# Kernel tuning notes

Measured on AMD Instinct MI355X. Metric: run time of the kernel, lower is better.

Reference implementation:

```python
import jax, jax.numpy as jnp
import numpy as np

N_QUBITS = 12
N_LAYERS = 6
BATCH = 8192
D_IN = 512


def _apply_1q(state, gate, wire):
    # state: [B] + [2]*n (real), gate: [2,2]. new[j] = sum_i gate[j,i]*old[i]
    s = jnp.moveaxis(state, 1 + wire, -1)
    s = jnp.einsum('...i,ji->...j', s, gate)
    return jnp.moveaxis(s, -1, 1 + wire)


def _apply_cnot(state, ctrl, tgt):
    # flip target amplitude pair where control bit == 1
    s = jnp.moveaxis(state, (1 + ctrl, 1 + tgt), (-2, -1))
    s = jnp.concatenate([s[..., :1, :], s[..., 1:, ::-1]], axis=-2)
    return jnp.moveaxis(s, (-2, -1), (1 + ctrl, 1 + tgt))


def _simulate(angles, weights):
    # angles: [B, n] per-sample RY angles; weights: [L, n] shared RY angles.
    # Circuit: H + RY(angle) per wire on |0>, then L x (RY layer + CNOT chain).
    # All gates are real -> real float32 statevector.
    B, n = angles.shape
    L = weights.shape[0]
    inv_sqrt2 = jnp.float32(1.0 / np.sqrt(2.0))
    half = 0.5 * angles
    c, s = jnp.cos(half), jnp.sin(half)
    # per-wire single-qubit state RY(a) @ H @ |0> = inv_sqrt2 * [c-s, c+s]
    v = inv_sqrt2 * jnp.stack([c - s, c + s], axis=-1)  # [B, n, 2]
    state = v[:, 0]  # [B, 2]
    for w in range(1, n):
        state = jnp.einsum('b...,bj->b...j', state, v[:, w])  # product state
    # state: [B] + [2]*n
    for layer in range(L):
        h = 0.5 * weights[layer]
        cl, sl = jnp.cos(h), jnp.sin(h)
        for w in range(n):
            gate = jnp.stack([jnp.stack([cl[w], -sl[w]]),
                              jnp.stack([sl[w], cl[w]])])
            state = _apply_1q(state, gate, w)
        for w in range(n - 1):
            state = _apply_cnot(state, w, w + 1)
    probs = state * state
    zs = []
    for w in range(n):
        axes = tuple(a for a in range(1, n + 1) if a != 1 + w)
        p = probs.sum(axis=axes)  # [B, 2]
        zs.append(p[:, 0] - p[:, 1])
    return jnp.stack(zs, axis=-1)  # [B, n] = <Z_i>


def setup_inputs() -> dict:
    key = jax.random.key(0)
    ks = jax.random.split(key, 6)
    x = jax.random.normal(ks[0], (BATCH, D_IN), jnp.float32)
    pre_w = jax.random.normal(ks[1], (N_QUBITS, D_IN), jnp.float32) / np.sqrt(D_IN)
    pre_b = jax.random.normal(ks[2], (N_QUBITS,), jnp.float32) * 0.01
    weights = jax.random.normal(ks[3], (N_LAYERS, N_QUBITS), jnp.float32)
    post_w = jax.random.normal(ks[4], (1, N_QUBITS), jnp.float32) / np.sqrt(N_QUBITS)
    post_b = jax.random.normal(ks[5], (1,), jnp.float32) * 0.01
    return {"x": x, "pre_w": pre_w, "pre_b": pre_b, "weights": weights,
            "post_w": post_w, "post_b": post_b}


def reference(x, pre_w, pre_b, weights, post_w, post_b):
    pre = x @ pre_w.T + pre_b                # [B, n_qubits]
    angles = pre * jnp.float32(np.pi / 2.0)  # RY(inputs[i]*pi/2)
    q_out = _simulate(angles, weights)       # [B, n_qubits]
    return q_out @ post_w.T + post_b         # [B, 1]
```

## Files before the change

kernel.cpp:

```cpp
#include <hip/hip_runtime.h>
#include <math.h>

#define NQ 12
#define NL 6
#define BATCHN 8192
#define DIN 512

typedef _Float16 f16;
typedef __attribute__((ext_vector_type(8)))  _Float16 f16x8;
typedef __attribute__((ext_vector_type(16))) float    f32x16;
typedef unsigned int u32;
typedef __attribute__((ext_vector_type(4))) u32 u32x4;
typedef __attribute__((ext_vector_type(2))) int i32x2;


__device__ __forceinline__ u32 pkrtz(float a, float b) {
  auto p = __builtin_amdgcn_cvt_pkrtz(a, b);
  return __builtin_bit_cast(u32, p);
}
__device__ __forceinline__ u32 bperm(int addr, u32 v) {
  return (u32)__builtin_amdgcn_ds_bpermute(addr, (int)v);
}
__device__ __forceinline__ float dppx1(float v) {
  return __int_as_float(__builtin_amdgcn_mov_dpp(__float_as_int(v), 0xB1, 0xF, 0xF, true));
}
__device__ __forceinline__ u32 dppx1u(u32 v) {
  return (u32)__builtin_amdgcn_mov_dpp((int)v, 0xB1, 0xF, 0xF, true);
}
__device__ __forceinline__ float dppx2(float v) {
  return __int_as_float(__builtin_amdgcn_mov_dpp(__float_as_int(v), 0x4E, 0xF, 0xF, true));
}
__device__ __forceinline__ float dppx8(float v) {
  return __int_as_float(__builtin_amdgcn_mov_dpp(__float_as_int(v), 0x128, 0xF, 0xF, true));
}
template <int PAT>
__device__ __forceinline__ float swzf(float v) {
  return __int_as_float(__builtin_amdgcn_ds_swizzle(__float_as_int(v), PAT));
}
__device__ __forceinline__ float wave_sum(float v) {
  v += dppx1(v);
  v += dppx2(v);
  v += swzf<0x101F>(v);
  v += dppx8(v);
  v += swzf<0x401F>(v);
  v += __shfl_xor(v, 32, 64);
  return v;
}
__device__ __forceinline__ f16x8 asf(const u32 a[4]) {
  u32x4 v; v.x = a[0]; v.y = a[1]; v.z = a[2]; v.w = a[3];
  return __builtin_bit_cast(f16x8, v);
}
__device__ __forceinline__ f16x8 ldB(const u32* __restrict__ p, int off) {
  u32x4 v = *(const u32x4*)(p + off);
  return __builtin_bit_cast(f16x8, v);
}

__device__ __forceinline__ void sincos_rev(float rev, float* s, float* c) {
  float r = rev - floorf(rev);
#if __has_builtin(__builtin_amdgcn_sinf) && __has_builtin(__builtin_amdgcn_cosf)
  *s = __builtin_amdgcn_sinf(r);
  *c = __builtin_amdgcn_cosf(r);
#else
  const float TWO_PI = 6.28318530717958647693f;
  sincosf(r * TWO_PI, s, c);
#endif
}

#if __has_builtin(__builtin_amdgcn_permlane32_swap)
__device__ __forceinline__ void pswap(u32& a, u32& b) {
  i32x2 r = __builtin_amdgcn_permlane32_swap((int)a, (int)b, false, false);
  a = (u32)r.x; b = (u32)r.y;
}
#else
#define PSWAP_FALLBACK 1
__device__ __forceinline__ void pswap_fb(u32& a, u32& b, bool hi, int axor) {
  u32 xa = bperm(axor, a), xb = bperm(axor, b);
  u32 na = hi ? xb : a;
  u32 nb = hi ? b : xa;
  a = na; b = nb;
}
#endif

__device__ __forceinline__ u32 foldw(u32 w, u32 m) {
  u32 partner = dppx1u(w);
  return (m & partner) | (~m & w);
}

__global__ void setup_mats(const float* __restrict__ weights, u32* __restrict__ Bbuf) {
  const int mm = blockIdx.x >> 3;
  const int l  = mm >> 1;
  const int qs = mm & 1;
  __shared__ float c6[6], s6[6];
  if (threadIdx.x < 6) {
    float h = 0.5f * weights[l * NQ + qs * 6 + threadIdx.x];
    c6[threadIdx.x] = cosf(h);
    s6[threadIdx.x] = sinf(h);
  }
  __syncthreads();
  const int t = (blockIdx.x & 7) * 256 + threadIdx.x;
  const int lane = (t >> 2) & 63;
  const int fk   = t >> 8;
  const int kt   = fk & 3;
  const int nt   = fk >> 2;
  const int n     = nt * 32 + (lane & 31);
  const int kbase = kt * 16 + (lane >> 5) * 8 + (t & 3) * 2;
  float v[2];
  #pragma unroll
  for (int u = 0; u < 2; ++u) {
    int k = kbase + u;
    int bb = k;
    if (l >= 1) { bb ^= bb << 1; bb ^= bb << 2; bb ^= bb << 4; bb &= 63; }
    float prod = 1.f;
    #pragma unroll
    for (int w = 0; w < 6; ++w) {
      const int aw = (n >> w) & 1, bw = (bb >> w) & 1;
      prod *= (aw == bw) ? c6[w] : (aw ? s6[w] : -s6[w]);
    }
    v[u] = prod;
  }
  Bbuf[mm * 2048 + t] = pkrtz(v[0], v[1]);
}

template <bool FOLD>
__device__ __forceinline__ void mm_step(f32x16 (&d)[2][2], const u32* __restrict__ Bl,
                                        bool hi, int axor, u32 maskA, u32 maskB) {
  f16x8 B[2][4];
  #pragma unroll
  for (int kt = 0; kt < 4; ++kt) {
    B[0][kt] = ldB(Bl, (0 * 4 + kt) * 256);
    B[1][kt] = ldB(Bl, (1 * 4 + kt) * 256);
  }
  u32 fr[2][4][4];
  #pragma unroll
  for (int kt = 0; kt < 4; ++kt) {
    const int s  = kt >> 1;
    const int b0 = 4 * ((2 * kt) & 3);
    const int b1 = 4 * ((2 * kt + 1) & 3);
    #pragma unroll
    for (int mt = 0; mt < 2; ++mt) {
      u32 p0a = pkrtz(d[s][mt][b0 + 0], d[s][mt][b0 + 1]);
      u32 p0b = pkrtz(d[s][mt][b0 + 2], d[s][mt][b0 + 3]);
      u32 p1a = pkrtz(d[s][mt][b1 + 0], d[s][mt][b1 + 1]);
      u32 p1b = pkrtz(d[s][mt][b1 + 2], d[s][mt][b1 + 3]);
      if (FOLD) {
        const int PAR4[4] = {0, 1, 1, 0};
        const int ka = (PAR4[b0 >> 2] + s) & 1;
        const int kc = (PAR4[b1 >> 2] + s) & 1;
        p0a = foldw(p0a, ka ? maskB : maskA);
        p0b = foldw(p0b, ka ? maskA : maskB);
        p1a = foldw(p1a, kc ? maskB : maskA);
        p1b = foldw(p1b, kc ? maskA : maskB);
      }
#ifdef PSWAP_FALLBACK
      pswap_fb(p0a, p1a, hi, axor);
      pswap_fb(p0b, p1b, hi, axor);
#else
      pswap(p0a, p1a);
      pswap(p0b, p1b);
#endif
      fr[mt][kt][0] = p0a;
      fr[mt][kt][1] = p0b;
      fr[mt][kt][2] = p1a;
      fr[mt][kt][3] = p1b;
    }
  }
  #pragma unroll
  for (int kt = 0; kt < 4; ++kt) {
    f16x8 A0 = asf(fr[0][kt]);
    f16x8 A1 = asf(fr[1][kt]);
    if (kt == 0) {
      f32x16 z{};
      d[0][0] = __builtin_amdgcn_mfma_f32_32x32x16_f16(A0, B[0][kt], z, 0, 0, 0);
      d[0][1] = __builtin_amdgcn_mfma_f32_32x32x16_f16(A0, B[1][kt], z, 0, 0, 0);
      d[1][0] = __builtin_amdgcn_mfma_f32_32x32x16_f16(A1, B[0][kt], z, 0, 0, 0);
      d[1][1] = __builtin_amdgcn_mfma_f32_32x32x16_f16(A1, B[1][kt], z, 0, 0, 0);
    } else {
      d[0][0] = __builtin_amdgcn_mfma_f32_32x32x16_f16(A0, B[0][kt], d[0][0], 0, 0, 0);
      d[0][1] = __builtin_amdgcn_mfma_f32_32x32x16_f16(A0, B[1][kt], d[0][1], 0, 0, 0);
      d[1][0] = __builtin_amdgcn_mfma_f32_32x32x16_f16(A1, B[0][kt], d[1][0], 0, 0, 0);
      d[1][1] = __builtin_amdgcn_mfma_f32_32x32x16_f16(A1, B[1][kt], d[1][1], 0, 0, 0);
    }
  }
}

__global__ void __launch_bounds__(256) __attribute__((amdgpu_waves_per_eu(3, 4)))
dqc_main(const float* __restrict__ x,
         const float* __restrict__ pre_w,
         const float* __restrict__ pre_b,
         const float* __restrict__ weights,
         const float* __restrict__ post_w,
         const float* __restrict__ post_b,
         const u32* __restrict__ Bbuf,
         float* __restrict__ out)
{
  const int lane = threadIdx.x & 63;
  const bool hi  = lane >= 32;
  const int b    = blockIdx.x * 4 + (threadIdx.x >> 6);
  const int axor = (lane ^ 32) << 2;
  const u32 maskA = hi ? 0x0000FFFFu : 0xFFFF0000u;
  const u32 maskB = ~maskA;

  float acc[NQ];
  const float* xr = x + (size_t)b * DIN + lane * 8;
  const float4 xa = *(const float4*)(xr);
  const float4 xb = *(const float4*)(xr + 4);
  #pragma unroll
  for (int w = 0; w < NQ; ++w) {
    const float* wr = pre_w + w * DIN + lane * 8;
    const float4 wa = *(const float4*)(wr);
    const float4 wb = *(const float4*)(wr + 4);
    acc[w] = xa.x * wa.x + xa.y * wa.y + xa.z * wa.z + xa.w * wa.w
           + xb.x * wb.x + xb.y * wb.y + xb.z * wb.z + xb.w * wb.w;
  }
  #pragma unroll
  for (int w = 0; w < NQ; ++w) acc[w] = wave_sum(acc[w]);

  const float INV_4PI = 0.07957747154594766788f;
  float u0[NQ], u1[NQ];
  #pragma unroll
  for (int w = 0; w < NQ; ++w) {
    const float cw2 = 0.125f + pre_b[w] * 0.125f + weights[w] * INV_4PI;
    const float rev = fmaf(acc[w], 0.125f, cw2);
    sincos_rev(rev, &u1[w], &u0[w]);
  }

  float base8[8];
  #pragma unroll
  for (int j = 0; j < 8; ++j)
    base8[j] = ((j & 1) ? u1[0] : u0[0]) * ((j & 2) ? u1[1] : u0[1]) * ((j & 4) ? u1[2] : u0[2]);
  float hiP[4];
  #pragma unroll
  for (int kt = 0; kt < 4; ++kt)
    hiP[kt] = (hi ? u1[3] : u0[3]) * ((kt & 1) ? u1[4] : u0[4]) * ((kt & 2) ? u1[5] : u0[5]);
  const float q5 = ((lane & 2) ? u1[7] : u0[7]) * ((lane & 4) ? u1[8] : u0[8])
                 * ((lane & 8) ? u1[9] : u0[9]) * ((lane & 16) ? u1[10] : u0[10]);
  const float qA = q5 * ((lane & 1) ? u1[6] : u0[6]);
  const float qB = q5 * ((lane & 1) ? u0[6] : u1[6]);
  const float qeven = hi ? qB : qA;
  const float qodd  = hi ? qA : qB;
  const float qe0 = qeven * u0[11], qo0 = qodd * u0[11];
  const float qe1 = qeven * u1[11], qo1 = qodd * u1[11];

  f32x16 d[2][2];
  {
    const u32* Bl = Bbuf + 2 * 2048 + lane * 4;
    const int PKT[4] = {0, 1, 1, 0};
    const int PDW[4] = {0, 1, 1, 0};
    #pragma unroll
    for (int kt = 0; kt < 4; ++kt) {
      u32 a0[4], a1[4];
      #pragma unroll
      for (int dw = 0; dw < 4; ++dw) {
        const float e0 = base8[2 * dw] * hiP[kt];
        const float e1 = base8[2 * dw + 1] * hiP[kt];
        const bool cls = (PKT[kt] ^ PDW[dw]) != 0;
        a0[dw] = pkrtz((cls ? qo0 : qe0) * e0, (cls ? qe0 : qo0) * e1);
        a1[dw] = pkrtz((cls ? qo1 : qe1) * e0, (cls ? qe1 : qo1) * e1);
      }
      f16x8 A0 = asf(a0), A1 = asf(a1);
      f16x8 B0 = ldB(Bl, (0 * 4 + kt) * 256);
      f16x8 B1 = ldB(Bl, (1 * 4 + kt) * 256);
      if (kt == 0) {
        f32x16 z{};
        d[0][0] = __builtin_amdgcn_mfma_f32_32x32x16_f16(A0, B0, z, 0, 0, 0);
        d[0][1] = __builtin_amdgcn_mfma_f32_32x32x16_f16(A0, B1, z, 0, 0, 0);
        d[1][0] = __builtin_amdgcn_mfma_f32_32x32x16_f16(A1, B0, z, 0, 0, 0);
        d[1][1] = __builtin_amdgcn_mfma_f32_32x32x16_f16(A1, B1, z, 0, 0, 0);
      } else {
        d[0][0] = __builtin_amdgcn_mfma_f32_32x32x16_f16(A0, B0, d[0][0], 0, 0, 0);
        d[0][1] = __builtin_amdgcn_mfma_f32_32x32x16_f16(A0, B1, d[0][1], 0, 0, 0);
        d[1][0] = __builtin_amdgcn_mfma_f32_32x32x16_f16(A1, B0, d[1][0], 0, 0, 0);
        d[1][1] = __builtin_amdgcn_mfma_f32_32x32x16_f16(A1, B1, d[1][1], 0, 0, 0);
      }
    }
  }

  #pragma unroll
  for (int i = 0; i < 4; ++i) {
    mm_step<false>(d, Bbuf + (2 * i + 3) * 2048 + lane * 4, hi, axor, maskA, maskB);
    mm_step<true >(d, Bbuf + (2 * i + 4) * 2048 + lane * 4, hi, axor, maskA, maskB);
  }
  mm_step<false>(d, Bbuf + 11 * 2048 + lane * 4, hi, axor, maskA, maskB);

  const float pw0 = post_w[0], pw1 = post_w[1], pw2 = post_w[2],
              pw3 = post_w[3], pw4 = post_w[4], pw5 = post_w[5];
  float A0s = 0.f, A1s = 0.f, s00 = 0.f, s01 = 0.f, accA = 0.f, accB = 0.f;
  #pragma unroll
  for (int mt = 0; mt < 2; ++mt)
    #pragma unroll
    for (int nt = 0; nt < 2; ++nt)
      #pragma unroll
      for (int r = 0; r < 16; ++r) {
        float v = d[mt][nt][r];
        float sq = v * v;
        const int par0 = (__builtin_popcount(r & 3) + __builtin_popcount(r >> 2) + mt) & 1;
        if (par0) A1s += sq; else A0s += sq;
        if (nt == 0) { if (par0) s01 += sq; else s00 += sq; }
        const int c0 = r & 1;
        const int c1 = (r ^ (r >> 1)) & 1;
        const int c3 = c1 ^ ((r >> 2) & 1);
        const int c4 = c3 ^ ((r >> 3) & 1);
        const int c5 = c4 ^ mt;
        const float ca = (c0 ? -pw0 : pw0) + (c1 ? -pw1 : pw1);
        const float cb = (c1 ? -pw2 : pw2) + (c3 ? -pw3 : pw3)
                       + (c4 ? -pw4 : pw4) + (c5 ? -pw5 : pw5);
        accA = fmaf(ca, sq, accA);
        accB = fmaf(cb, sq, accB);
      }
  const float sgnhi = hi ? -1.f : 1.f;
  const float tot   = A0s + A1s;
  const float diff  = sgnhi * (A0s - A1s);
  const float diffs = sgnhi * (2.f * (s00 - s01) - (A0s - A1s));
  float Sq = 0.f;
  #pragma unroll
  for (int j = 0; j < 5; ++j) {
    const int par = __builtin_popcount(lane & ((2 << j) - 1)) & 1;
    Sq += par ? -post_w[6 + j] : post_w[6 + j];
  }
  const float s5 = (__builtin_popcount(lane & 31) & 1) ? -post_w[11] : post_w[11];
  const float zcomb = accA + sgnhi * accB + diff * Sq + diffs * s5;

  const float tots = wave_sum(tot);
  const float zs   = wave_sum(zcomb);

  if (lane == 0) {
    out[b] = fmaf(zs, 1.0f / tots, post_b[0]);
  }
}

extern "C" void kernel_launch(void* const* d_in, const int* in_sizes, int n_in,
                              void* d_out, int out_size, void* d_ws, size_t ws_size,
                              hipStream_t stream) {
  (void)in_sizes; (void)n_in; (void)out_size; (void)ws_size;
  const float* x       = (const float*)d_in[0];
  const float* pre_w   = (const float*)d_in[1];
  const float* pre_b   = (const float*)d_in[2];
  const float* weights = (const float*)d_in[3];
  const float* post_w  = (const float*)d_in[4];
  const float* post_b  = (const float*)d_in[5];
  float* out = (float*)d_out;
  u32* Bbuf = (u32*)d_ws;

  setup_mats<<<96, 256, 0, stream>>>(weights, Bbuf);
  dqc_main<<<BATCHN / 4, 256, 0, stream>>>(x, pre_w, pre_b, weights,
                                           post_w, post_b, Bbuf, out);
}
```

Baseline: 115.1 us.

## Ping-pong MFMA accumulators across layer steps and interleave A-fragment packing with MFMAs

Splits the state accumulator into two ping-pong register sets so each matrix step reads one set and writes the other. Fragment packing is now interleaved per k-tile with the MFMAs rather than done fully in advance, so conversion work can overlap matrix-core execution. It also lowers the waves-per-EU minimum from 3 to 2 so the compiler may use more registers, and replaces the final cross-half shuffle in wave_sum with permlane32_swap. The extra accumulator set raises register pressure and may reduce occupancy.

```diff
diff --git a/kernel.cpp b/kernel.cpp
--- a/kernel.cpp
+++ b/kernel.cpp
@@ -37,14 +37,35 @@
 __device__ __forceinline__ float swzf(float v) {
   return __int_as_float(__builtin_amdgcn_ds_swizzle(__float_as_int(v), PAT));
 }
+
+#if __has_builtin(__builtin_amdgcn_permlane32_swap)
+__device__ __forceinline__ void pswap(u32& a, u32& b) {
+  i32x2 r = __builtin_amdgcn_permlane32_swap((int)a, (int)b, false, false);
+  a = (u32)r.x; b = (u32)r.y;
+}
+#else
+#define PSWAP_FALLBACK 1
+__device__ __forceinline__ void pswap_fb(u32& a, u32& b, bool hi, int axor) {
+  u32 xa = bperm(axor, a), xb = bperm(axor, b);
+  u32 na = hi ? xb : a;
+  u32 nb = hi ? b : xa;
+  a = na; b = nb;
+}
+#endif
+
 __device__ __forceinline__ float wave_sum(float v) {
   v += dppx1(v);
   v += dppx2(v);
   v += swzf<0x101F>(v);
   v += dppx8(v);
   v += swzf<0x401F>(v);
-  v += __shfl_xor(v, 32, 64);
-  return v;
+#ifndef PSWAP_FALLBACK
+  u32 a = __builtin_bit_cast(u32, v), b = a;
+  pswap(a, b);
+  return __builtin_bit_cast(float, a) + __builtin_bit_cast(float, b);
+#else
+  return v + __shfl_xor(v, 32, 64);
+#endif
 }
 __device__ __forceinline__ f16x8 asf(const u32 a[4]) {
   u32x4 v; v.x = a[0]; v.y = a[1]; v.z = a[2]; v.w = a[3];
@@ -65,21 +86,6 @@
   sincosf(r * TWO_PI, s, c);
 #endif
 }
-
-#if __has_builtin(__builtin_amdgcn_permlane32_swap)
-__device__ __forceinline__ void pswap(u32& a, u32& b) {
-  i32x2 r = __builtin_amdgcn_permlane32_swap((int)a, (int)b, false, false);
-  a = (u32)r.x; b = (u32)r.y;
-}
-#else
-#define PSWAP_FALLBACK 1
-__device__ __forceinline__ void pswap_fb(u32& a, u32& b, bool hi, int axor) {
-  u32 xa = bperm(axor, a), xb = bperm(axor, b);
-  u32 na = hi ? xb : a;
-  u32 nb = hi ? b : xa;
-  a = na; b = nb;
-}
-#endif
 
 __device__ __forceinline__ u32 foldw(u32 w, u32 m) {
   u32 partner = dppx1u(w);
@@ -122,26 +128,28 @@
 }
 
 template <bool FOLD>
-__device__ __forceinline__ void mm_step(f32x16 (&d)[2][2], const u32* __restrict__ Bl,
+__device__ __forceinline__ void mm_step(const f32x16 (&din)[2][2], f32x16 (&dout)[2][2],
+                                        const u32* __restrict__ Bl,
                                         bool hi, int axor, u32 maskA, u32 maskB) {
+  (void)hi; (void)axor;
   f16x8 B[2][4];
   #pragma unroll
   for (int kt = 0; kt < 4; ++kt) {
     B[0][kt] = ldB(Bl, (0 * 4 + kt) * 256);
     B[1][kt] = ldB(Bl, (1 * 4 + kt) * 256);
   }
-  u32 fr[2][4][4];
   #pragma unroll
   for (int kt = 0; kt < 4; ++kt) {
     const int s  = kt >> 1;
     const int b0 = 4 * ((2 * kt) & 3);
     const int b1 = 4 * ((2 * kt + 1) & 3);
+    f16x8 A[2];
     #pragma unroll
     for (int mt = 0; mt < 2; ++mt) {
-      u32 p0a = pkrtz(d[s][mt][b0 + 0], d[s][mt][b0 + 1]);
-      u32 p0b = pkrtz(d[s][mt][b0 + 2], d[s][mt][b0 + 3]);
-      u32 p1a = pkrtz(d[s][mt][b1 + 0], d[s][mt][b1 + 1]);
-      u32 p1b = pkrtz(d[s][mt][b1 + 2], d[s][mt][b1 + 3]);
+      u32 p0a = pkrtz(din[s][mt][b0 + 0], din[s][mt][b0 + 1]);
+      u32 p0b = pkrtz(din[s][mt][b0 + 2], din[s][mt][b0 + 3]);
+      u32 p1a = pkrtz(din[s][mt][b1 + 0], din[s][mt][b1 + 1]);
+      u32 p1b = pkrtz(din[s][mt][b1 + 2], din[s][mt][b1 + 3]);
       if (FOLD) {
         const int PAR4[4] = {0, 1, 1, 0};
         const int ka = (PAR4[b0 >> 2] + s) & 1;
@@ -158,32 +166,25 @@
       pswap(p0a, p1a);
       pswap(p0b, p1b);
 #endif
-      fr[mt][kt][0] = p0a;
-      fr[mt][kt][1] = p0b;
-      fr[mt][kt][2] = p1a;
-      fr[mt][kt][3] = p1b;
+      u32 w[4] = {p0a, p0b, p1a, p1b};
+      A[mt] = asf(w);
     }
-  }
-  #pragma unroll
-  for (int kt = 0; kt < 4; ++kt) {
-    f16x8 A0 = asf(fr[0][kt]);
-    f16x8 A1 = asf(fr[1][kt]);
     if (kt == 0) {
       f32x16 z{};
-      d[0][0] = __builtin_amdgcn_mfma_f32_32x32x16_f16(A0, B[0][kt], z, 0, 0, 0);
-      d[0][1] = __builtin_amdgcn_mfma_f32_32x32x16_f16(A0, B[1][kt], z, 0, 0, 0);
-      d[1][0] = __builtin_amdgcn_mfma_f32_32x32x16_f16(A1, B[0][kt], z, 0, 0, 0);
-      d[1][1] = __builtin_amdgcn_mfma_f32_32x32x16_f16(A1, B[1][kt], z, 0, 0, 0);
+      dout[0][0] = __builtin_amdgcn_mfma_f32_32x32x16_f16(A[0], B[0][0], z, 0, 0, 0);
+      dout[0][1] = __builtin_amdgcn_mfma_f32_32x32x16_f16(A[0], B[1][0], z, 0, 0, 0);
+      dout[1][0] = __builtin_amdgcn_mfma_f32_32x32x16_f16(A[1], B[0][0], z, 0, 0, 0);
+      dout[1][1] = __builtin_amdgcn_mfma_f32_32x32x16_f16(A[1], B[1][0], z, 0, 0, 0);
     } else {
-      d[0][0] = __builtin_amdgcn_mfma_f32_32x32x16_f16(A0, B[0][kt], d[0][0], 0, 0, 0);
-      d[0][1] = __builtin_amdgcn_mfma_f32_32x32x16_f16(A0, B[1][kt], d[0][1], 0, 0, 0);
-      d[1][0] = __builtin_amdgcn_mfma_f32_32x32x16_f16(A1, B[0][kt], d[1][0], 0, 0, 0);
-      d[1][1] = __builtin_amdgcn_mfma_f32_32x32x16_f16(A1, B[1][kt], d[1][1], 0, 0, 0);
+      dout[0][0] = __builtin_amdgcn_mfma_f32_32x32x16_f16(A[0], B[0][kt], dout[0][0], 0, 0, 0);
+      dout[0][1] = __builtin_amdgcn_mfma_f32_32x32x16_f16(A[0], B[1][kt], dout[0][1], 0, 0, 0);
+      dout[1][0] = __builtin_amdgcn_mfma_f32_32x32x16_f16(A[1], B[0][kt], dout[1][0], 0, 0, 0);
+      dout[1][1] = __builtin_amdgcn_mfma_f32_32x32x16_f16(A[1], B[1][kt], dout[1][1], 0, 0, 0);
     }
   }
 }
 
-__global__ void __launch_bounds__(256) __attribute__((amdgpu_waves_per_eu(3, 4)))
+__global__ void __launch_bounds__(256) __attribute__((amdgpu_waves_per_eu(2, 4)))
 dqc_main(const float* __restrict__ x,
          const float* __restrict__ pre_w,
          const float* __restrict__ pre_b,
@@ -241,7 +242,7 @@
   const float qe0 = qeven * u0[11], qo0 = qodd * u0[11];
   const float qe1 = qeven * u1[11], qo1 = qodd * u1[11];
 
-  f32x16 d[2][2];
+  f32x16 dA[2][2], dB[2][2];
   {
     const u32* Bl = Bbuf + 2 * 2048 + lane * 4;
     const int PKT[4] = {0, 1, 1, 0};
@@ -262,25 +263,25 @@
       f16x8 B1 = ldB(Bl, (1 * 4 + kt) * 256);
       if (kt == 0) {
         f32x16 z{};
-        d[0][0] = __builtin_amdgcn_mfma_f32_32x32x16_f16(A0, B0, z, 0, 0, 0);
-        d[0][1] = __builtin_amdgcn_mfma_f32_32x32x16_f16(A0, B1, z, 0, 0, 0);
-        d[1][0] = __builtin_amdgcn_mfma_f32_32x32x16_f16(A1, B0, z, 0, 0, 0);
-        d[1][1] = __builtin_amdgcn_mfma_f32_32x32x16_f16(A1, B1, z, 0, 0, 0);
+        dA[0][0] = __builtin_amdgcn_mfma_f32_32x32x16_f16(A0, B0, z, 0, 0, 0);
+        dA[0][1] = __builtin_amdgcn_mfma_f32_32x32x16_f16(A0, B1, z, 0, 0, 0);
+        dA[1][0] = __builtin_amdgcn_mfma_f32_32x32x16_f16(A1, B0, z, 0, 0, 0);
+        dA[1][1] = __builtin_amdgcn_mfma_f32_32x32x16_f16(A1, B1, z, 0, 0, 0);
       } else {
-        d[0][0] = __builtin_amdgcn_mfma_f32_32x32x16_f16(A0, B0, d[0][0], 0, 0, 0);
-        d[0][1] = __builtin_amdgcn_mfma_f32_32x32x16_f16(A0, B1, d[0][1], 0, 0, 0);
-        d[1][0] = __builtin_amdgcn_mfma_f32_32x32x16_f16(A1, B0, d[1][0], 0, 0, 0);
-        d[1][1] = __builtin_amdgcn_mfma_f32_32x32x16_f16(A1, B1, d[1][1], 0, 0, 0);
+        dA[0][0] = __builtin_amdgcn_mfma_f32_32x32x16_f16(A0, B0, dA[0][0], 0, 0, 0);
+        dA[0][1] = __builtin_amdgcn_mfma_f32_32x32x16_f16(A0, B1, dA[0][1], 0, 0, 0);
+        dA[1][0] = __builtin_amdgcn_mfma_f32_32x32x16_f16(A1, B0, dA[1][0], 0, 0, 0);
+        dA[1][1] = __builtin_amdgcn_mfma_f32_32x32x16_f16(A1, B1, dA[1][1], 0, 0, 0);
       }
     }
   }
 
   #pragma unroll
   for (int i = 0; i < 4; ++i) {
-    mm_step<false>(d, Bbuf + (2 * i + 3) * 2048 + lane * 4, hi, axor, maskA, maskB);
-    mm_step<true >(d, Bbuf + (2 * i + 4) * 2048 + lane * 4, hi, axor, maskA, maskB);
-  }
-  mm_step<false>(d, Bbuf + 11 * 2048 + lane * 4, hi, axor, maskA, maskB);
+    mm_step<false>(dA, dB, Bbuf + (2 * i + 3) * 2048 + lane * 4, hi, axor, maskA, maskB);
+    mm_step<true >(dB, dA, Bbuf + (2 * i + 4) * 2048 + lane * 4, hi, axor, maskA, maskB);
+  }
+  mm_step<false>(dA, dB, Bbuf + 11 * 2048 + lane * 4, hi, axor, maskA, maskB);
 
   const float pw0 = post_w[0], pw1 = post_w[1], pw2 = post_w[2],
               pw3 = post_w[3], pw4 = post_w[4], pw5 = post_w[5];
@@ -291,7 +292,7 @@
     for (int nt = 0; nt < 2; ++nt)
       #pragma unroll
       for (int r = 0; r < 16; ++r) {
-        float v = d[mt][nt][r];
+        float v = dB[mt][nt][r];
         float sq = v * v;
         const int par0 = (__builtin_popcount(r & 3) + __builtin_popcount(r >> 2) + mt) & 1;
         if (par0) A1s += sq; else A0s += sq;
```

Result: slower. 118.4 us (+2.9%).

## Double-buffer B matrix loads across MFMA steps and use permlane32 swap in reduction

Applied to the files above, without the earlier changes.

Each layer's B fragments are now prefetched one step ahead into ping-pong register buffers, and the first two sets are issued before the wave reduction. This hides global/L2 load latency behind the MFMA and repack work. The last stage of the wave sum uses permlane32_swap instead of a shuffle. The cost is more live vector registers, which may lower occupancy or cause spills. The fallback path now passes hi=false and axor=0 to pswap_fb, which looks wrong if that path is compiled.

```diff
diff --git a/kernel.cpp b/kernel.cpp
--- a/kernel.cpp
+++ b/kernel.cpp
@@ -37,14 +37,35 @@
 __device__ __forceinline__ float swzf(float v) {
   return __int_as_float(__builtin_amdgcn_ds_swizzle(__float_as_int(v), PAT));
 }
+
+#if __has_builtin(__builtin_amdgcn_permlane32_swap)
+__device__ __forceinline__ void pswap(u32& a, u32& b) {
+  i32x2 r = __builtin_amdgcn_permlane32_swap((int)a, (int)b, false, false);
+  a = (u32)r.x; b = (u32)r.y;
+}
+#else
+#define PSWAP_FALLBACK 1
+__device__ __forceinline__ void pswap_fb(u32& a, u32& b, bool hi, int axor) {
+  u32 xa = bperm(axor, a), xb = bperm(axor, b);
+  u32 na = hi ? xb : a;
+  u32 nb = hi ? b : xa;
+  a = na; b = nb;
+}
+#endif
+
 __device__ __forceinline__ float wave_sum(float v) {
   v += dppx1(v);
   v += dppx2(v);
   v += swzf<0x101F>(v);
   v += dppx8(v);
   v += swzf<0x401F>(v);
-  v += __shfl_xor(v, 32, 64);
-  return v;
+#ifndef PSWAP_FALLBACK
+  u32 a = __builtin_bit_cast(u32, v), b = a;
+  pswap(a, b);
+  return __builtin_bit_cast(float, a) + __builtin_bit_cast(float, b);
+#else
+  return v + __shfl_xor(v, 32, 64);
+#endif
 }
 __device__ __forceinline__ f16x8 asf(const u32 a[4]) {
   u32x4 v; v.x = a[0]; v.y = a[1]; v.z = a[2]; v.w = a[3];
@@ -53,6 +74,13 @@
 __device__ __forceinline__ f16x8 ldB(const u32* __restrict__ p, int off) {
   u32x4 v = *(const u32x4*)(p + off);
   return __builtin_bit_cast(f16x8, v);
+}
+__device__ __forceinline__ void loadB(f16x8 (&B)[2][4], const u32* __restrict__ Bl) {
+  #pragma unroll
+  for (int kt = 0; kt < 4; ++kt) {
+    B[0][kt] = ldB(Bl, (0 * 4 + kt) * 256);
+    B[1][kt] = ldB(Bl, (1 * 4 + kt) * 256);
+  }
 }
 
 __device__ __forceinline__ void sincos_rev(float rev, float* s, float* c) {
@@ -65,21 +93,6 @@
   sincosf(r * TWO_PI, s, c);
 #endif
 }
-
-#if __has_builtin(__builtin_amdgcn_permlane32_swap)
-__device__ __forceinline__ void pswap(u32& a, u32& b) {
-  i32x2 r = __builtin_amdgcn_permlane32_swap((int)a, (int)b, false, false);
-  a = (u32)r.x; b = (u32)r.y;
-}
-#else
-#define PSWAP_FALLBACK 1
-__device__ __forceinline__ void pswap_fb(u32& a, u32& b, bool hi, int axor) {
-  u32 xa = bperm(axor, a), xb = bperm(axor, b);
-  u32 na = hi ? xb : a;
-  u32 nb = hi ? b : xa;
-  a = na; b = nb;
-}
-#endif
 
 __device__ __forceinline__ u32 foldw(u32 w, u32 m) {
   u32 partner = dppx1u(w);
@@ -121,14 +134,14 @@
   Bbuf[mm * 2048 + t] = pkrtz(v[0], v[1]);
 }
 
-template <bool FOLD>
-__device__ __forceinline__ void mm_step(f32x16 (&d)[2][2], const u32* __restrict__ Bl,
-                                        bool hi, int axor, u32 maskA, u32 maskB) {
-  f16x8 B[2][4];
-  #pragma unroll
-  for (int kt = 0; kt < 4; ++kt) {
-    B[0][kt] = ldB(Bl, (0 * 4 + kt) * 256);
-    B[1][kt] = ldB(Bl, (1 * 4 + kt) * 256);
+template <bool FOLD, bool PRE>
+__device__ __forceinline__ void mm_step(f32x16 (&d)[2][2],
+                                        const f16x8 (&B)[2][4],
+                                        f16x8 (&Bn)[2][4],
+                                        const u32* __restrict__ Bln,
+                                        u32 maskA, u32 maskB) {
+  if constexpr (PRE) {
+    loadB(Bn, Bln);
   }
   u32 fr[2][4][4];
   #pragma unroll
@@ -152,8 +165,8 @@
         p1b = foldw(p1b, kc ? maskA : maskB);
       }
 #ifdef PSWAP_FALLBACK
-      pswap_fb(p0a, p1a, hi, axor);
-      pswap_fb(p0b, p1b, hi, axor);
+      pswap_fb(p0a, p1a, false, 0);
+      pswap_fb(p0b, p1b, false, 0);
 #else
       pswap(p0a, p1a);
       pswap(p0b, p1b);
@@ -196,7 +209,6 @@
   const int lane = threadIdx.x & 63;
   const bool hi  = lane >= 32;
   const int b    = blockIdx.x * 4 + (threadIdx.x >> 6);
-  const int axor = (lane ^ 32) << 2;
   const u32 maskA = hi ? 0x0000FFFFu : 0xFFFF0000u;
   const u32 maskB = ~maskA;
 
@@ -212,6 +224,12 @@
     acc[w] = xa.x * wa.x + xa.y * wa.y + xa.z * wa.z + xa.w * wa.w
            + xb.x * wb.x + xb.y * wb.y + xb.z * wb.z + xb.w * wb.w;
   }
+
+  const u32* BlBase = Bbuf + lane * 4;
+  f16x8 Ba[2][4], Bb[2][4];
+  loadB(Ba, BlBase + 2 * 2048);
+  loadB(Bb, BlBase + 3 * 2048);
+
   #pragma unroll
   for (int w = 0; w < NQ; ++w) acc[w] = wave_sum(acc[w]);
 
@@ -243,7 +261,6 @@
 
   f32x16 d[2][2];
   {
-    const u32* Bl = Bbuf + 2 * 2048 + lane * 4;
     const int PKT[4] = {0, 1, 1, 0};
     const int PDW[4] = {0, 1, 1, 0};
     #pragma unroll
@@ -258,29 +275,27 @@
         a1[dw] = pkrtz((cls ? qo1 : qe1) * e0, (cls ? qe1 : qo1) * e1);
       }
       f16x8 A0 = asf(a0), A1 = asf(a1);
-      f16x8 B0 = ldB(Bl, (0 * 4 + kt) * 256);
-      f16x8 B1 = ldB(Bl, (1 * 4 + kt) * 256);
       if (kt == 0) {
         f32x16 z{};
-        d[0][0] = __builtin_amdgcn_mfma_f32_32x32x16_f16(A0, B0, z, 0, 0, 0);
-        d[0][1] = __builtin_amdgcn_mfma_f32_32x32x16_f16(A0, B1, z, 0, 0, 0);
-        d[1][0] = __builtin_amdgcn_mfma_f32_32x32x16_f16(A1, B0, z, 0, 0, 0);
-        d[1][1] = __builtin_amdgcn_mfma_f32_32x32x16_f16(A1, B1, z, 0, 0, 0);
+        d[0][0] = __builtin_amdgcn_mfma_f32_32x32x16_f16(A0, Ba[0][kt], z, 0, 0, 0);
+        d[0][1] = __builtin_amdgcn_mfma_f32_32x32x16_f16(A0, Ba[1][kt], z, 0, 0, 0);
+        d[1][0] = __builtin_amdgcn_mfma_f32_32x32x16_f16(A1, Ba[0][kt], z, 0, 0, 0);
+        d[1][1] = __builtin_amdgcn_mfma_f32_32x32x16_f16(A1, Ba[1][kt], z, 0, 0, 0);
       } else {
-        d[0][0] = __builtin_amdgcn_mfma_f32_32x32x16_f16(A0, B0, d[0][0], 0, 0, 0);
-        d[0][1] = __builtin_amdgcn_mfma_f32_32x32x16_f16(A0, B1, d[0][1], 0, 0, 0);
-        d[1][0] = __builtin_amdgcn_mfma_f32_32x32x16_f16(A1, B0, d[1][0], 0, 0, 0);
-        d[1][1] = __builtin_amdgcn_mfma_f32_32x32x16_f16(A1, B1, d[1][1], 0, 0, 0);
+        d[0][0] = __builtin_amdgcn_mfma_f32_32x32x16_f16(A0, Ba[0][kt], d[0][0], 0, 0, 0);
+        d[0][1] = __builtin_amdgcn_mfma_f32_32x32x16_f16(A0, Ba[1][kt], d[0][1], 0, 0, 0);
+        d[1][0] = __builtin_amdgcn_mfma_f32_32x32x16_f16(A1, Ba[0][kt], d[1][0], 0, 0, 0);
+        d[1][1] = __builtin_amdgcn_mfma_f32_32x32x16_f16(A1, Ba[1][kt], d[1][1], 0, 0, 0);
       }
     }
   }
 
   #pragma unroll
   for (int i = 0; i < 4; ++i) {
-    mm_step<false>(d, Bbuf + (2 * i + 3) * 2048 + lane * 4, hi, axor, maskA, maskB);
-    mm_step<true >(d, Bbuf + (2 * i + 4) * 2048 + lane * 4, hi, axor, maskA, maskB);
-  }
-  mm_step<false>(d, Bbuf + 11 * 2048 + lane * 4, hi, axor, maskA, maskB);
+    mm_step<false, true>(d, Bb, Ba, BlBase + (2 * i + 4) * 2048, maskA, maskB);
+    mm_step<true,  true>(d, Ba, Bb, BlBase + (2 * i + 5) * 2048, maskA, maskB);
+  }
+  mm_step<false, false>(d, Bb, Ba, nullptr, maskA, maskB);
 
   const float pw0 = post_w[0], pw1 = post_w[1], pw2 = post_w[2],
               pw3 = post_w[3], pw4 = post_w[4], pw5 = post_w[5];
```

New measurement: 116.1 us. About the same (+0.8%).

## Stream B fragments per k-step and raise occupancy target to cut register pressure

Applied to the files above, without the earlier changes.

Each matrix step now loads its B-operand fragments one k-tile ahead inside the MFMA loop, instead of preloading all eight fragments up front. This lowers live VGPRs, and the waves-per-EU hint is raised from (3,4) to (4,8) so more waves can run per EU. The cross-half wave reduction in wave_sum now uses permlane32_swap instead of a shuffle. The cost is that B-load latency is hidden by less lookahead, and the compiler may spill if the new occupancy target is too tight. The fallback pswap path now passes hi=false and axor=0, which would be wrong, but it only builds when permlane32_swap is unavailable.

```diff
diff --git a/kernel.cpp b/kernel.cpp
--- a/kernel.cpp
+++ b/kernel.cpp
@@ -37,14 +37,35 @@
 __device__ __forceinline__ float swzf(float v) {
   return __int_as_float(__builtin_amdgcn_ds_swizzle(__float_as_int(v), PAT));
 }
+
+#if __has_builtin(__builtin_amdgcn_permlane32_swap)
+__device__ __forceinline__ void pswap(u32& a, u32& b) {
+  i32x2 r = __builtin_amdgcn_permlane32_swap((int)a, (int)b, false, false);
+  a = (u32)r.x; b = (u32)r.y;
+}
+#else
+#define PSWAP_FALLBACK 1
+__device__ __forceinline__ void pswap_fb(u32& a, u32& b, bool hi, int axor) {
+  u32 xa = bperm(axor, a), xb = bperm(axor, b);
+  u32 na = hi ? xb : a;
+  u32 nb = hi ? b : xa;
+  a = na; b = nb;
+}
+#endif
+
 __device__ __forceinline__ float wave_sum(float v) {
   v += dppx1(v);
   v += dppx2(v);
   v += swzf<0x101F>(v);
   v += dppx8(v);
   v += swzf<0x401F>(v);
-  v += __shfl_xor(v, 32, 64);
-  return v;
+#ifndef PSWAP_FALLBACK
+  u32 a = __builtin_bit_cast(u32, v), b = a;
+  pswap(a, b);
+  return __builtin_bit_cast(float, a) + __builtin_bit_cast(float, b);
+#else
+  return v + __shfl_xor(v, 32, 64);
+#endif
 }
 __device__ __forceinline__ f16x8 asf(const u32 a[4]) {
   u32x4 v; v.x = a[0]; v.y = a[1]; v.z = a[2]; v.w = a[3];
@@ -66,21 +87,6 @@
 #endif
 }
 
-#if __has_builtin(__builtin_amdgcn_permlane32_swap)
-__device__ __forceinline__ void pswap(u32& a, u32& b) {
-  i32x2 r = __builtin_amdgcn_permlane32_swap((int)a, (int)b, false, false);
-  a = (u32)r.x; b = (u32)r.y;
-}
-#else
-#define PSWAP_FALLBACK 1
-__device__ __forceinline__ void pswap_fb(u32& a, u32& b, bool hi, int axor) {
-  u32 xa = bperm(axor, a), xb = bperm(axor, b);
-  u32 na = hi ? xb : a;
-  u32 nb = hi ? b : xa;
-  a = na; b = nb;
-}
-#endif
-
 __device__ __forceinline__ u32 foldw(u32 w, u32 m) {
   u32 partner = dppx1u(w);
   return (m & partner) | (~m & w);
@@ -122,14 +128,11 @@
 }
 
 template <bool FOLD>
-__device__ __forceinline__ void mm_step(f32x16 (&d)[2][2], const u32* __restrict__ Bl,
-                                        bool hi, int axor, u32 maskA, u32 maskB) {
-  f16x8 B[2][4];
-  #pragma unroll
-  for (int kt = 0; kt < 4; ++kt) {
-    B[0][kt] = ldB(Bl, (0 * 4 + kt) * 256);
-    B[1][kt] = ldB(Bl, (1 * 4 + kt) * 256);
-  }
+__device__ __forceinline__ void mm_step(f32x16 (&d)[2][2],
+                                        const u32* __restrict__ Bl,
+                                        u32 maskA, u32 maskB) {
+  f16x8 Bc0 = ldB(Bl, 0 * 256);
+  f16x8 Bc1 = ldB(Bl, 4 * 256);
   u32 fr[2][4][4];
   #pragma unroll
   for (int kt = 0; kt < 4; ++kt) {
@@ -152,8 +155,8 @@
         p1b = foldw(p1b, kc ? maskA : maskB);
       }
 #ifdef PSWAP_FALLBACK
-      pswap_fb(p0a, p1a, hi, axor);
-      pswap_fb(p0b, p1b, hi, axor);
+      pswap_fb(p0a, p1a, false, 0);
+      pswap_fb(p0b, p1b, false, 0);
 #else
       pswap(p0a, p1a);
       pswap(p0b, p1b);
@@ -166,24 +169,29 @@
   }
   #pragma unroll
   for (int kt = 0; kt < 4; ++kt) {
+    f16x8 B0 = Bc0, B1 = Bc1;
+    if (kt < 3) {
+      Bc0 = ldB(Bl, (kt + 1) * 256);
+      Bc1 = ldB(Bl, (4 + kt + 1) * 256);
+    }
     f16x8 A0 = asf(fr[0][kt]);
     f16x8 A1 = asf(fr[1][kt]);
     if (kt == 0) {
       f32x16 z{};
-      d[0][0] = __builtin_amdgcn_mfma_f32_32x32x16_f16(A0, B[0][kt], z, 0, 0, 0);
-      d[0][1] = __builtin_amdgcn_mfma_f32_32x32x16_f16(A0, B[1][kt], z, 0, 0, 0);
-      d[1][0] = __builtin_amdgcn_mfma_f32_32x32x16_f16(A1, B[0][kt], z, 0, 0, 0);
-      d[1][1] = __builtin_amdgcn_mfma_f32_32x32x16_f16(A1, B[1][kt], z, 0, 0, 0);
+      d[0][0] = __builtin_amdgcn_mfma_f32_32x32x16_f16(A0, B0, z, 0, 0, 0);
+      d[0][1] = __builtin_amdgcn_mfma_f32_32x32x16_f16(A0, B1, z, 0, 0, 0);
+      d[1][0] = __builtin_amdgcn_mfma_f32_32x32x16_f16(A1, B0, z, 0, 0, 0);
+      d[1][1] = __builtin_amdgcn_mfma_f32_32x32x16_f16(A1, B1, z, 0, 0, 0);
     } else {
-      d[0][0] = __builtin_amdgcn_mfma_f32_32x32x16_f16(A0, B[0][kt], d[0][0], 0, 0, 0);
-      d[0][1] = __builtin_amdgcn_mfma_f32_32x32x16_f16(A0, B[1][kt], d[0][1], 0, 0, 0);
-      d[1][0] = __builtin_amdgcn_mfma_f32_32x32x16_f16(A1, B[0][kt], d[1][0], 0, 0, 0);
-      d[1][1] = __builtin_amdgcn_mfma_f32_32x32x16_f16(A1, B[1][kt], d[1][1], 0, 0, 0);
-    }
-  }
-}
-
-__global__ void __launch_bounds__(256) __attribute__((amdgpu_waves_per_eu(3, 4)))
+      d[0][0] = __builtin_amdgcn_mfma_f32_32x32x16_f16(A0, B0, d[0][0], 0, 0, 0);
+      d[0][1] = __builtin_amdgcn_mfma_f32_32x32x16_f16(A0, B1, d[0][1], 0, 0, 0);
+      d[1][0] = __builtin_amdgcn_mfma_f32_32x32x16_f16(A1, B0, d[1][0], 0, 0, 0);
+      d[1][1] = __builtin_amdgcn_mfma_f32_32x32x16_f16(A1, B1, d[1][1], 0, 0, 0);
+    }
+  }
+}
+
+__global__ void __launch_bounds__(256) __attribute__((amdgpu_waves_per_eu(4, 8)))
 dqc_main(const float* __restrict__ x,
          const float* __restrict__ pre_w,
          const float* __restrict__ pre_b,
@@ -196,7 +204,6 @@
   const int lane = threadIdx.x & 63;
   const bool hi  = lane >= 32;
   const int b    = blockIdx.x * 4 + (threadIdx.x >> 6);
-  const int axor = (lane ^ 32) << 2;
   const u32 maskA = hi ? 0x0000FFFFu : 0xFFFF0000u;
   const u32 maskB = ~maskA;
 
@@ -241,9 +248,13 @@
   const float qe0 = qeven * u0[11], qo0 = qodd * u0[11];
   const float qe1 = qeven * u1[11], qo1 = qodd * u1[11];
 
+  const u32* BlBase = Bbuf + lane * 4;
+
   f32x16 d[2][2];
   {
-    const u32* Bl = Bbuf + 2 * 2048 + lane * 4;
+    const u32* Bl2 = BlBase + 2 * 2048;
+    f16x8 Ic0 = ldB(Bl2, 0 * 256);
+    f16x8 Ic1 = ldB(Bl2, 4 * 256);
     const int PKT[4] = {0, 1, 1, 0};
     const int PDW[4] = {0, 1, 1, 0};
     #pragma unroll
@@ -257,9 +268,12 @@
         a0[dw] = pkrtz((cls ? qo0 : qe0) * e0, (cls ? qe0 : qo0) * e1);
         a1[dw] = pkrtz((cls ? qo1 : qe1) * e0, (cls ? qe1 : qo1) * e1);
       }
+      f16x8 B0 = Ic0, B1 = Ic1;
+      if (kt < 3) {
+        Ic0 = ldB(Bl2, (kt + 1) * 256);
+        Ic1 = ldB(Bl2, (4 + kt + 1) * 256);
+      }
       f16x8 A0 = asf(a0), A1 = asf(a1);
-      f16x8 B0 = ldB(Bl, (0 * 4 + kt) * 256);
-      f16x8 B1 = ldB(Bl, (1 * 4 + kt) * 256);
       if (kt == 0) {
         f32x16 z{};
         d[0][0] = __builtin_amdgcn_mfma_f32_32x32x16_f16(A0, B0, z, 0, 0, 0);
@@ -277,10 +291,10 @@
 
   #pragma unroll
   for (int i = 0; i < 4; ++i) {
-    mm_step<false>(d, Bbuf + (2 * i + 3) * 2048 + lane * 4, hi, axor, maskA, maskB);
-    mm_step<true >(d, Bbuf + (2 * i + 4) * 2048 + lane * 4, hi, axor, maskA, maskB);
-  }
-  mm_step<false>(d, Bbuf + 11 * 2048 + lane * 4, hi, axor, maskA, maskB);
+    mm_step<false>(d, BlBase + (2 * i + 3) * 2048, maskA, maskB);
+    mm_step<true >(d, BlBase + (2 * i + 4) * 2048, maskA, maskB);
+  }
+  mm_step<false>(d, BlBase + 11 * 2048, maskA, maskB);
 
   const float pw0 = post_w[0], pw1 = post_w[1], pw2 = post_w[2],
               pw3 = post_w[3], pw4 = post_w[4], pw5 = post_w[5];
```

Result: no change. 117.0 us (+1.7%).
